# Kernel tuning notes

Measured on AMD Instinct MI355X. Metric: run time of the kernel, lower is better.

The kernel has to match this reference:

```python
import jax, jax.numpy as jnp
import numpy as np
from jax import lax

B, D, N, K, POOL = 256, 512, 50000, 32, 1024
ALPHA, BETA, LAMB = 1.0, 1.0, 1e-4
TAU, EPS, DELTA = 0.1, 0.1, 1e-3
SINKHORN_ITERS = 200


def matrix_sqrt(A):
    # differentiable symmetric PSD matrix sqrt via eigendecomposition
    w, v = jnp.linalg.eigh(A)
    w = jnp.clip(w, 0.0)
    return (v * jnp.sqrt(w)) @ v.T


def ridge_cov(M, delta):
    Dm = M.shape[0]
    S = M + (jnp.trace(M) / Dm * delta) * jnp.eye(Dm, dtype=M.dtype)
    return 0.5 * (S + S.T)


def sinkhorn(p, q, C, eps):
    # entropic OT, fixed-iteration Sinkhorn (ot.sinkhorn equivalent)
    Kmat = jnp.exp(-C / eps)
    def step(uv, _):
        u, v = uv
        u = p / (Kmat @ v + 1e-16)
        v = q / (Kmat.T @ u + 1e-16)
        return (u, v), None
    (u, v), _ = lax.scan(step, (jnp.ones_like(p), jnp.ones_like(q)), None, length=SINKHORN_ITERS)
    return u[:, None] * Kmat * v[None, :]


def setup_inputs():
    key = jax.random.key(0)
    k1, k2, k3, k4, k5, k6 = jax.random.split(key, 6)
    return {
        "q_batch": jax.random.normal(k1, (B, D), jnp.float32),
        "q_indices": jax.random.randint(k2, (B,), 0, POOL),
        "W": jax.random.normal(k3, (D, D), jnp.float32) * 0.05,
        "X": jax.random.normal(k4, (N, D), jnp.float32),
        "pre_indices": jax.random.randint(k5, (POOL, K), 0, N),
        "pre_weights": jax.random.uniform(k6, (POOL, K), jnp.float32, 0.1, 1.0),
    }


def _forward(q_batch, W, X, pre_weights, q_indices, pre_indices):
    T = q_batch @ W  # model := single linear layer, T_q_batch [B, D]
    # ---- distribution alignment (2-Wasserstein between Gaussians) ----
    mu_X = X.mean(0)
    Sigma_X = ridge_cov(jnp.cov(X, rowvar=False).astype(X.dtype), DELTA)
    mu_t = T.mean(0)
    Sigma_t = ridge_cov(jnp.cov(T, rowvar=False).astype(T.dtype), max(DELTA, 1e-4))
    term_mean = jnp.sum((mu_t - mu_X) ** 2)
    s_t = matrix_sqrt(Sigma_t)
    M = s_t @ Sigma_X @ s_t
    s_m = matrix_sqrt(0.5 * (M + M.T))
    term_cov = jnp.trace(Sigma_X + Sigma_t - 2.0 * s_m)
    loss_dist = term_mean + jnp.clip(term_cov, 0.0)
    # ---- kNN consistency with entropic OT ----
    T_sg = lax.stop_gradient(T)  # faiss search is on detached queries
    d2 = (T_sg ** 2).sum(1, keepdims=True) - 2.0 * T_sg @ X.T + (X ** 2).sum(1)[None, :]
    _, post_idx = lax.top_k(-d2, K)  # exact brute-force kNN == faiss IndexFlatL2
    Xn = X[post_idx]  # [B, K, D]
    l2 = ((T[:, None, :] - Xn) ** 2).sum(-1)  # [B, K], grads flow through T
    post_w = jax.nn.softmax(-l2 / TAU, axis=1)
    post_w = jnp.clip(post_w, 1e-8)
    post_w = post_w / post_w.sum(1, keepdims=True)
    pre_idx_b = pre_indices[q_indices]  # [B, K]
    pre_w = jnp.clip(pre_weights[q_indices], 1e-8)
    pre_w = pre_w / pre_w.sum(1, keepdims=True)
    # fixed-size support = concat(pre, post) of size 2K; duplicated points cost 0
    # to move between, so OT value matches the deduped-union formulation
    support = jnp.concatenate([pre_idx_b, post_idx], axis=1)  # [B, 2K]
    S = X[support]  # [B, 2K, D]
    sq = (S ** 2).sum(-1)
    C = jnp.clip(sq[:, :, None] + sq[:, None, :] - 2.0 * jnp.einsum('bid,bjd->bij', S, S), 0.0)
    med = jnp.median(C.reshape(C.shape[0], -1), axis=1)
    C = C / (med[:, None, None] + 1e-8)
    zeros = jnp.zeros_like(pre_w)
    p = jnp.concatenate([pre_w, zeros], axis=1)   # pre mass on first K slots
    q = jnp.concatenate([zeros, post_w], axis=1)  # post mass on last K slots
    plans = jax.vmap(lambda pp, qq, cc: sinkhorn(pp, qq, cc, EPS))(p, q, C)
    loss_knn = (plans * C).sum((1, 2)).mean()
    loss_reg = 0.5 * jnp.sum(W ** 2)
    total = ALPHA * loss_dist + BETA * loss_knn + LAMB * loss_reg
    return total, loss_dist, loss_knn


def reference(q_batch, q_indices, W, X, pre_indices, pre_weights):
    return _forward(q_batch, W, X, pre_weights, q_indices, pre_indices)
```

## Files before the change

### kernel.cpp

```cpp
#include <hip/hip_runtime.h>
#include <float.h>
#include <math.h>

#define BB 256
#define DD 512
#define NN 50000
#define KK 32
#define NS_ITERS 11
#define PARTS 8
#define PCH 6250

#define OFF_G     0
#define OFF_SC    262144
#define OFF_CS    262208
#define OFF_CSS   262720
#define ZERO_F    263232
#define OFF_T     263232
#define OFF_TC    394304
#define OFF_P     525376
#define OFF_H     656448
#define OFF_XSQ   723008
#define OFF_RUNI  781200
#define OFF_PW    789392
#define OFF_PRW   797584
#define OFF_D2    805776

#define OFF_UUT   (OFF_G)
#define OFF_TCTC  (OFF_G + 65536)
#define OFF_W     (OFF_G + 131072)
#define OFF_M     (OFF_G + 131328)
#define OFF_MUT   (OFF_G + 200000)

typedef __attribute__((ext_vector_type(8))) short bf16x8;
typedef __attribute__((ext_vector_type(4))) float f32x4;

__device__ __forceinline__ float waveSum(float v) {
#pragma unroll
  for (int off = 32; off > 0; off >>= 1) v += __shfl_xor(v, off);
  return v;
}

__device__ __forceinline__ void cvt_write(float4 v, unsigned short* hi, unsigned short* lo, int sa) {
  unsigned int b0 = __float_as_uint(v.x), b1 = __float_as_uint(v.y);
  unsigned int b2 = __float_as_uint(v.z), b3 = __float_as_uint(v.w);
  unsigned int h0 = b0 & 0xffff0000u, h1 = b1 & 0xffff0000u;
  unsigned int h2 = b2 & 0xffff0000u, h3 = b3 & 0xffff0000u;
  float l0 = v.x - __uint_as_float(h0), l1 = v.y - __uint_as_float(h1);
  float l2 = v.z - __uint_as_float(h2), l3 = v.w - __uint_as_float(h3);
  *(unsigned int*)&hi[sa]     = (h0 >> 16) | h1;
  *(unsigned int*)&hi[sa + 2] = (h2 >> 16) | h3;
  *(unsigned int*)&lo[sa]     = (__float_as_uint(l0) >> 16) | (__float_as_uint(l1) & 0xffff0000u);
  *(unsigned int*)&lo[sa + 2] = (__float_as_uint(l2) >> 16) | (__float_as_uint(l3) & 0xffff0000u);
}

__device__ __forceinline__ void cvt1(float x, unsigned short* hp, unsigned short* lp) {
// ... 150 lines not shown
      }
#pragma unroll
      for (int nj = 0; nj < 4; ++nj) {
        int ro = (n0 + nj * 16 + lrow) * 72 + kb;
        bh[nj] = *(const bf16x8*)&Bh[ro];
        bl[nj] = *(const bf16x8*)&Bl[ro];
      }
#pragma unroll
      for (int mi = 0; mi < 4; ++mi)
#pragma unroll
        for (int nj = 0; nj < 4; ++nj) {
          acc[mi][nj] = __builtin_amdgcn_mfma_f32_16x16x32_bf16(ah[mi], bh[nj], acc[mi][nj], 0, 0, 0);
          acc[mi][nj] = __builtin_amdgcn_mfma_f32_16x16x32_bf16(ah[mi], bl[nj], acc[mi][nj], 0, 0, 0);
          acc[mi][nj] = __builtin_amdgcn_mfma_f32_16x16x32_bf16(al[mi], bh[nj], acc[mi][nj], 0, 0, 0);
        }
    }
    __syncthreads();
  }
  if (t < 128) colpart[t] = 0.f;
  __syncthreads();
#pragma unroll
  for (int mi = 0; mi < 4; ++mi)
#pragma unroll
    for (int nj = 0; nj < 4; ++nj)
#pragma unroll
      for (int r = 0; r < 4; ++r) {
        int row = bi * 128 + m0 + mi * 16 + lq * 4 + r;
        int col = bj * 128 + n0 + nj * 16 + lrow;
        if (col < NN) V[(size_t)row * NN + col] = acc[mi][nj][r];
      }
#pragma unroll
  for (int nj = 0; nj < 4; ++nj) {
    float s = 0.f;
#pragma unroll
    for (int mi = 0; mi < 4; ++mi)
#pragma unroll
      for (int r = 0; r < 4; ++r) s += acc[mi][nj][r];
    atomicAdd(&colpart[n0 + nj * 16 + lrow], s);
  }
  __syncthreads();
  if (t < 128) {
    int col = bj * 128 + t;
    if (col < NN) atomicAdd(&m[col], colpart[t] * (1.0f / 256.0f));
  }
}

__global__ void __launch_bounds__(256) k_uut(const float* __restrict__ V,
                                             const float* __restrict__ m,
                                             float* __restrict__ UUT) {
  __shared__ unsigned short Ah[128 * 72], Al[128 * 72], Bh[128 * 72], Bl[128 * 72];
  __shared__ __align__(16) float ms[1000];
  const int pi_[3] = {0, 0, 1}, pj_[3] = {0, 1, 1};
  int bi = pi_[blockIdx.x], bj = pj_[blockIdx.x];
  int j0 = blockIdx.y * 1000, jlim = j0 + 1000;
  int t = threadIdx.x;
  int wave = t >> 6, lane = t & 63;
  int m0 = (wave >> 1) * 64, n0 = (wave & 1) * 64;
  int lrow = lane & 15, lq = lane >> 4;
  int r_ = t >> 4, c4_ = (t & 15) * 4;
  f32x4 acc[4][4] = {};
  if (t < 250) ((float4*)ms)[t] = *(const float4*)&m[j0 + t * 4];
  float4 pa[8], pb[8];
#pragma unroll
  for (int f = 0; f < 8; ++f) {
    int r = f * 16 + r_;
    int jb = j0 + c4_;
    float4 va = {0.f, 0.f, 0.f, 0.f}, vb = {0.f, 0.f, 0.f, 0.f};
    if (jb < jlim) {
      va = *(const float4*)&V[(size_t)(bi * 128 + r) * NN + jb];
      vb = *(const float4*)&V[(size_t)(bj * 128 + r) * NN + jb];
    }
    pa[f] = va; pb[f] = vb;
  }
  __syncthreads();
  for (int ch = 0; ch < 16; ++ch) {
    int jc = j0 + ch * 64;
#pragma unroll
    for (int f = 0; f < 8; ++f) {
      int sa = (f * 16 + r_) * 72 + c4_;
      int jb = jc + c4_;
      float4 va = pa[f], vb = pb[f];
      if (jb < jlim) {
        float4 mm = *(const float4*)&ms[jb - j0];
        va.x -= mm.x; va.y -= mm.y; va.z -= mm.z; va.w -= mm.w;
        vb.x -= mm.x; vb.y -= mm.y; vb.z -= mm.z; vb.w -= mm.w;
      }
      cvt_write(va, Ah, Al, sa);
      cvt_write(vb, Bh, Bl, sa);
    }
    __syncthreads();
    if (ch < 15) {
      int jn = j0 + (ch + 1) * 64;
#pragma unroll
      for (int f = 0; f < 8; ++f) {
        int r = f * 16 + r_;
        int jb = jn + c4_;
        float4 va = {0.f, 0.f, 0.f, 0.f}, vb = {0.f, 0.f, 0.f, 0.f};
        if (jb < jlim) {
          va = *(const float4*)&V[(size_t)(bi * 128 + r) * NN + jb];
          vb = *(const float4*)&V[(size_t)(bj * 128 + r) * NN + jb];
        }
        pa[f] = va; pb[f] = vb;
      }
    }
#pragma unroll
    for (int ks = 0; ks < 2; ++ks) {
      int kb = ks * 32 + lq * 8;
      bf16x8 ah[4], al[4], bh[4], bl[4];
#pragma unroll
      for (int mi = 0; mi < 4; ++mi) {
        int ro = (m0 + mi * 16 + lrow) * 72 + kb;
        ah[mi] = *(const bf16x8*)&Ah[ro];
        al[mi] = *(const bf16x8*)&Al[ro];
      }
#pragma unroll
      for (int nj = 0; nj < 4; ++nj) {
        int ro = (n0 + nj * 16 + lrow) * 72 + kb;
        bh[nj] = *(const bf16x8*)&Bh[ro];
        bl[nj] = *(const bf16x8*)&Bl[ro];
      }
#pragma unroll
      for (int mi = 0; mi < 4; ++mi)
#pragma unroll
        for (int nj = 0; nj < 4; ++nj) {
          acc[mi][nj] = __builtin_amdgcn_mfma_f32_16x16x32_bf16(ah[mi], bh[nj], acc[mi][nj], 0, 0, 0);
          acc[mi][nj] = __builtin_amdgcn_mfma_f32_16x16x32_bf16(ah[mi], bl[nj], acc[mi][nj], 0, 0, 0);
          acc[mi][nj] = __builtin_amdgcn_mfma_f32_16x16x32_bf16(al[mi], bh[nj], acc[mi][nj], 0, 0, 0);
        }
    }
    __syncthreads();
  }
#pragma unroll
  for (int mi = 0; mi < 4; ++mi)
#pragma unroll
    for (int nj = 0; nj < 4; ++nj)
#pragma unroll
      for (int r = 0; r < 4; ++r) {
        int row = bi * 128 + m0 + mi * 16 + lq * 4 + r;
        int col = bj * 128 + n0 + nj * 16 + lrow;
        atomicAdd(&UUT[row * 256 + col], acc[mi][nj][r]);
      }
}

__global__ void __launch_bounds__(256) k_colstatX(const float* __restrict__ X, float* __restrict__ colsum,
                                                  float* __restrict__ colss, float* __restrict__ xsq) {
  __shared__ float shs[512], shq[512];
  int b = blockIdx.x, t = threadIdx.x;
  int wave = t >> 6, lane = t & 63;
  shs[t] = 0.f; shq[t] = 0.f; shs[t + 256] = 0.f; shq[t + 256] = 0.f;
  __syncthreads();
  int c0 = lane * 4;
  float s0 = 0, s1 = 0, s2 = 0, s3 = 0, s4 = 0, s5 = 0, s6 = 0, s7 = 0;
  float q0 = 0, q1 = 0, q2 = 0, q3 = 0, q4 = 0, q5 = 0, q6 = 0, q7 = 0;
  int r0 = b * 200 + wave * 50;
  for (int rr = 0; rr < 50; ++rr) {
    const float* Xr = X + (size_t)(r0 + rr) * 512;
    float4 a = *(const float4*)&Xr[c0];
    float4 c = *(const float4*)&Xr[c0 + 256];
    s0 += a.x; s1 += a.y; s2 += a.z; s3 += a.w;
    s4 += c.x; s5 += c.y; s6 += c.z; s7 += c.w;
    float ax = a.x * a.x, ay = a.y * a.y, az = a.z * a.z, aw = a.w * a.w;
    float cx = c.x * c.x, cy = c.y * c.y, cz = c.z * c.z, cw = c.w * c.w;
    q0 += ax; q1 += ay; q2 += az; q3 += aw;
    q4 += cx; q5 += cy; q6 += cz; q7 += cw;
    float rsq = waveSum(((ax + ay) + (az + aw)) + ((cx + cy) + (cz + cw)));
    if (lane == 0) xsq[r0 + rr] = rsq;
  }
  atomicAdd(&shs[c0 + 0], s0); atomicAdd(&shs[c0 + 1], s1);
  atomicAdd(&shs[c0 + 2], s2); atomicAdd(&shs[c0 + 3], s3);
  atomicAdd(&shs[c0 + 256], s4); atomicAdd(&shs[c0 + 257], s5);
  atomicAdd(&shs[c0 + 258], s6); atomicAdd(&shs[c0 + 259], s7);
  atomicAdd(&shq[c0 + 0], q0); atomicAdd(&shq[c0 + 1], q1);
// ... 67 lines not shown
  int l = blockIdx.x * 256 + threadIdx.x;
  int i = l >> 8, j = l & 255;
  float u = (i >= 128 && j < 128) ? UUT[j * 256 + i] : UUT[i * 256 + j];
  float rho = scal[1] * (1e-3f / 512.0f);
  float wm = scal[6] * (1.0f / 256.0f);
  float wi = w[i] - wm, wj = w[j] - wm;
  H[l] = (u - 50000.0f * wi * wj) * (1.0f / (49999.0f * 255.0f))
       + rho * TcTc[i * 256 + j] * (1.0f / 255.0f);
}

__global__ void __launch_bounds__(256) k_power(const float* __restrict__ H,
                                               float* __restrict__ scal) {
  __shared__ float v[256], nv[256], red[4];
  int t = threadIdx.x;
  float rt = scal[0] * (1.0f / 255.0f) * (1e-3f / 512.0f);
  v[t] = 1.0f;
  __syncthreads();
  float n2 = 256.0f, n3 = 256.0f;
  for (int it = 0; it < 3; ++it) {
    float s = rt * v[t];
    for (int j = 0; j < 256; ++j) s += H[j * 256 + t] * v[j];
    nv[t] = s;
    float ss = waveSum(s * s);
    if ((t & 63) == 0) red[t >> 6] = ss;
    __syncthreads();
    float norm2 = red[0] + red[1] + red[2] + red[3];
    if (it == 1) n2 = norm2;
    if (it == 2) n3 = norm2;
    v[t] = nv[t];
    __syncthreads();
  }
  float d = H[t * 256 + t] + rt;
#pragma unroll
  for (int off = 32; off > 0; off >>= 1) d = fmaxf(d, __shfl_xor(d, off));
  if ((t & 63) == 0) red[t >> 6] = d;
  __syncthreads();
  if (t == 0) {
    float lam = sqrtf(n3 / n2);
    float md = fmaxf(fmaxf(red[0], red[1]), fmaxf(red[2], red[3]));
    scal[5] = fmaxf(1.3f * lam, md);
  }
}

__global__ void k_nsinit(const float* __restrict__ H, const float* __restrict__ scal,
                         float* __restrict__ Y, float* __restrict__ Z) {
  int l = blockIdx.x * 256 + threadIdx.x;
  int i = l >> 8, j = l & 255;
  float rt = scal[0] * (1.0f / 255.0f) * (1e-3f / 512.0f);
  float inv = 1.0f / scal[5];
  Y[l] = (H[l] + ((i == j) ? rt : 0.f)) * inv;
  Z[l] = (i == j) ? 1.0f : 0.f;
}

__global__ void __launch_bounds__(256) k_nsp(const float* __restrict__ Z,
                                             const float* __restrict__ Y,
                                             float* __restrict__ P) {
  __shared__ unsigned short Ah[64 * 72], Al[64 * 72], Bh[64 * 72], Bl[64 * 72];
  int n0b = blockIdx.x * 64, m0b = blockIdx.y * 64;
  int t = threadIdx.x, wave = t >> 6, lane = t & 63;
  int m0 = (wave >> 1) * 32, n0 = (wave & 1) * 32;
  int lrow = lane & 15, lq = lane >> 4;
  f32x4 acc[2][2] = {};
  for (int k0 = 0; k0 < 256; k0 += 64) {
#pragma unroll
    for (int f = 0; f < 4; ++f) {
      int lin = f * 256 + t;
      int r = lin >> 4, c4 = (lin & 15) * 4;
      float4 va = *(const float4*)&Z[(m0b + r) * 256 + k0 + c4];
      cvt_write(va, Ah, Al, r * 72 + c4);
      float4 vb = *(const float4*)&Y[(k0 + r) * 256 + n0b + c4];
      cvt1(vb.x, &Bh[(c4 + 0) * 72 + r], &Bl[(c4 + 0) * 72 + r]);
      cvt1(vb.y, &Bh[(c4 + 1) * 72 + r], &Bl[(c4 + 1) * 72 + r]);
      cvt1(vb.z, &Bh[(c4 + 2) * 72 + r], &Bl[(c4 + 2) * 72 + r]);
      cvt1(vb.w, &Bh[(c4 + 3) * 72 + r], &Bl[(c4 + 3) * 72 + r]);
    }
    __syncthreads();
#pragma unroll
    for (int ks = 0; ks < 2; ++ks) {
      int kb = ks * 32 + lq * 8;
      bf16x8 ah[2], al2[2], bh[2], bl2[2];
#pragma unroll
      for (int mi = 0; mi < 2; ++mi) {
        int ro = (m0 + mi * 16 + lrow) * 72 + kb;
        ah[mi] = *(const bf16x8*)&Ah[ro];
        al2[mi] = *(const bf16x8*)&Al[ro];
      }
#pragma unroll
      for (int nj = 0; nj < 2; ++nj) {
        int ro = (n0 + nj * 16 + lrow) * 72 + kb;
        bh[nj] = *(const bf16x8*)&Bh[ro];
        bl2[nj] = *(const bf16x8*)&Bl[ro];
      }
#pragma unroll
      for (int mi = 0; mi < 2; ++mi)
#pragma unroll
        for (int nj = 0; nj < 2; ++nj) {
          acc[mi][nj] = __builtin_amdgcn_mfma_f32_16x16x32_bf16(ah[mi], bh[nj], acc[mi][nj], 0, 0, 0);
          acc[mi][nj] = __builtin_amdgcn_mfma_f32_16x16x32_bf16(ah[mi], bl2[nj], acc[mi][nj], 0, 0, 0);
          acc[mi][nj] = __builtin_amdgcn_mfma_f32_16x16x32_bf16(al2[mi], bh[nj], acc[mi][nj], 0, 0, 0);
        }
    }
    __syncthreads();
  }
#pragma unroll
  for (int mi = 0; mi < 2; ++mi)
#pragma unroll
    for (int nj = 0; nj < 2; ++nj)
#pragma unroll
      for (int r = 0; r < 4; ++r) {
        int row = m0b + m0 + mi * 16 + lq * 4 + r;
        int col = n0b + n0 + nj * 16 + lrow;
        P[row * 256 + col] = acc[mi][nj][r];
      }
}

__global__ void __launch_bounds__(256) k_nsu(const float* __restrict__ Y, const float* __restrict__ Z,
                                             const float* __restrict__ Pm,
                                             float* __restrict__ Yn, float* __restrict__ Zn) {
  __shared__ unsigned short Ah[64 * 72], Al[64 * 72], Bh[64 * 72], Bl[64 * 72];
  int zz = blockIdx.z;
  const float* A = zz ? Pm : Y;
  const float* B = zz ? Z : Pm;
  const float* D = zz ? Z : Y;
  float* O = zz ? Zn : Yn;
  int n0b = blockIdx.x * 64, m0b = blockIdx.y * 64;
  int t = threadIdx.x, wave = t >> 6, lane = t & 63;
  int m0 = (wave >> 1) * 32, n0 = (wave & 1) * 32;
  int lrow = lane & 15, lq = lane >> 4;
  f32x4 acc[2][2] = {};
  for (int k0 = 0; k0 < 256; k0 += 64) {
#pragma unroll
    for (int f = 0; f < 4; ++f) {
      int lin = f * 256 + t;
      int r = lin >> 4, c4 = (lin & 15) * 4;
      float4 va = *(const float4*)&A[(m0b + r) * 256 + k0 + c4];
      cvt_write(va, Ah, Al, r * 72 + c4);
      float4 vb = *(const float4*)&B[(k0 + r) * 256 + n0b + c4];
      cvt1(vb.x, &Bh[(c4 + 0) * 72 + r], &Bl[(c4 + 0) * 72 + r]);
      cvt1(vb.y, &Bh[(c4 + 1) * 72 + r], &Bl[(c4 + 1) * 72 + r]);
      cvt1(vb.z, &Bh[(c4 + 2) * 72 + r], &Bl[(c4 + 2) * 72 + r]);
      cvt1(vb.w, &Bh[(c4 + 3) * 72 + r], &Bl[(c4 + 3) * 72 + r]);
    }
    __syncthreads();
#pragma unroll
    for (int ks = 0; ks < 2; ++ks) {
      int kb = ks * 32 + lq * 8;
      bf16x8 ah[2], al2[2], bh[2], bl2[2];
#pragma unroll
      for (int mi = 0; mi < 2; ++mi) {
        int ro = (m0 + mi * 16 + lrow) * 72 + kb;
        ah[mi] = *(const bf16x8*)&Ah[ro];
        al2[mi] = *(const bf16x8*)&Al[ro];
      }
#pragma unroll
      for (int nj = 0; nj < 2; ++nj) {
        int ro = (n0 + nj * 16 + lrow) * 72 + kb;
        bh[nj] = *(const bf16x8*)&Bh[ro];
        bl2[nj] = *(const bf16x8*)&Bl[ro];
      }
#pragma unroll
      for (int mi = 0; mi < 2; ++mi)
#pragma unroll
        for (int nj = 0; nj < 2; ++nj) {
          acc[mi][nj] = __builtin_amdgcn_mfma_f32_16x16x32_bf16(ah[mi], bh[nj], acc[mi][nj], 0, 0, 0);
          acc[mi][nj] = __builtin_amdgcn_mfma_f32_16x16x32_bf16(ah[mi], bl2[nj], acc[mi][nj], 0, 0, 0);
          acc[mi][nj] = __builtin_amdgcn_mfma_f32_16x16x32_bf16(al2[mi], bh[nj], acc[mi][nj], 0, 0, 0);
        }
    }
    __syncthreads();
  }
#pragma unroll
  for (int mi = 0; mi < 2; ++mi)
#pragma unroll
    for (int nj = 0; nj < 2; ++nj)
#pragma unroll
      for (int r = 0; r < 4; ++r) {
        int row = m0b + m0 + mi * 16 + lq * 4 + r;
        int col = n0b + n0 + nj * 16 + lrow;
        int idx = row * 256 + col;
        O[idx] = 1.5f * D[idx] - 0.5f * acc[mi][nj][r];
      }
}

__global__ void k_ns_trace(const float* __restrict__ Y, float* __restrict__ scal) {
  __shared__ float red[4];
  int t = threadIdx.x;
  float v = Y[t * 256 + t];
  v = waveSum(v);
  if ((t & 63) == 0) red[t >> 6] = v;
  __syncthreads();
  if (t == 0) {
    float tr = red[0] + red[1] + red[2] + red[3];
    float rt = scal[0] * (1.0f / 255.0f) * (1e-3f / 512.0f);
    scal[2] = sqrtf(scal[5]) * tr + 256.0f * sqrtf(rt);
  }
}

__global__ void __launch_bounds__(256) k_topk_part(const float* __restrict__ V,
                                                   const float* __restrict__ xsq,
                                                   float* __restrict__ candv,
                                                   int* __restrict__ candi) {
  __shared__ float bufv[512];
  __shared__ int bufi[512];
  __shared__ int lcount;
  __shared__ float tvs;
  __shared__ int tis;
  int part = blockIdx.x, q = blockIdx.y, t = threadIdx.x;
  int base = part * PCH;
  int lane = t & 63;
  if (t == 0) { lcount = 0; tvs = FLT_MAX; tis = 0x7fffffff; }
  __syncthreads();
  const float* rowV = V + (size_t)q * NN + base;
  const float* xs = xsq + base;

  auto flush = [&]() {
    __syncthreads();
    int c = lcount;
    for (int s = c + t; s < 512; s += 256) { bufv[s] = FLT_MAX; bufi[s] = 0x7fffffff; }
    __syncthreads();
    for (int ssz = 2; ssz <= 512; ssz <<= 1) {
      for (int st = ssz >> 1; st > 0; st >>= 1) {
        int i = 2 * t - (t & (st - 1));
        int j = i + st;
        bool up = ((i & ssz) == 0);
        float a = bufv[i], b = bufv[j];
        int ai = bufi[i], bi2 = bufi[j];
        bool agtb = (a > b) || (a == b && ai > bi2);
        if (agtb == up) { bufv[i] = b; bufv[j] = a; bufi[i] = bi2; bufi[j] = ai; }
        __syncthreads();
      }
    }
    if (t == 0) { lcount = 32; tvs = bufv[31]; tis = bufi[31]; }
    __syncthreads();
  };

  int ntile = (PCH + 255) >> 8;
  for (int tile = 0; tile < ntile; ++tile) {
    int j = tile * 256 + t;
    float val = 0.f; int idx = 0;
    bool pred = false;
    if (j < PCH) {
      val = xs[j] - 2.0f * rowV[j];
      idx = base + j;
      float tv = tvs; int ti = tis;
      pred = (val < tv) || (val == tv && idx < ti);
    }
    unsigned long long mask = __ballot(pred);
// ... 50 lines not shown
                                                const float* __restrict__ prew, float* __restrict__ postw,
                                                float* __restrict__ prewn) {
  __shared__ float l2s[32];
  int b = blockIdx.x, t = threadIdx.x;
  int wave = t >> 6, lane = t & 63;
  int qi = qidx[b];
  if (wave == 0) {
    float pwv = (lane < 32) ? fmaxf(prew[qi * 32 + lane], 1e-8f) : 0.f;
    float psum = waveSum(pwv);
    if (lane < 32) prewn[b * 32 + lane] = pwv / psum;
  }
  const float* Tb = T + b * 512;
#pragma unroll
  for (int n8 = 0; n8 < 8; ++n8) {
    int n = wave * 8 + n8;
    int nb = runi[b * 32 + n];
    const float* Xr = X + (size_t)nb * 512;
    float acc = 0.f;
#pragma unroll
    for (int d = 0; d < 8; ++d) {
      float df = Tb[lane + 64 * d] - Xr[lane + 64 * d];
      acc += df * df;
    }
    acc = waveSum(acc);
    if (lane == 0) l2s[n] = acc;
  }
  __syncthreads();
  if (wave == 0) {
    float lg = (lane < 32) ? (-l2s[lane] * 10.0f) : -FLT_MAX;
    float mx = lg;
#pragma unroll
    for (int off = 32; off > 0; off >>= 1) mx = fmaxf(mx, __shfl_xor(mx, off));
    float e = (lane < 32) ? expf(lg - mx) : 0.f;
    float es = waveSum(e);
    float wv = e / es;
    wv = fmaxf(wv, 1e-8f);
    float ws2 = (lane < 32) ? wv : 0.f;
    ws2 = waveSum(ws2);
    if (lane < 32) postw[b * 32 + lane] = wv / ws2;
  }
}

__global__ void __launch_bounds__(256) k_batch(const float* __restrict__ X, const int* __restrict__ qidx,
                                               const int* __restrict__ pre_idx, const int* __restrict__ runi,
                                               const float* __restrict__ prewn, const float* __restrict__ postw,
                                               float* __restrict__ scal) {
  __shared__ float G[64][65];
  __shared__ float Cm[64][65];
  __shared__ unsigned short Ah[64 * 72], Al[64 * 72];
  __shared__ int supp[64];
  __shared__ float uuS[32], vvS[32];
  __shared__ float red[4];
  __shared__ float medsh;
  __shared__ unsigned int cw[4], mw[4];
  int b = blockIdx.x, t = threadIdx.x;
  int wave = t >> 6, lane = t & 63;
  if (t < 32) supp[t] = pre_idx[qidx[b] * 32 + t];
  else if (t < 64) supp[t] = runi[b * 32 + t - 32];
  __syncthreads();
  {
    int m0 = (wave >> 1) * 32, n0 = (wave & 1) * 32;
    int lrow = lane & 15, lq = lane >> 4;
    int r_ = t >> 4, c4_ = (t & 15) * 4;
    f32x4 acc[2][2] = {};
    float4 pf[4];
#pragma unroll
    for (int f = 0; f < 4; ++f) {
      int r = f * 16 + r_;
      pf[f] = *(const float4*)&X[(size_t)supp[r] * 512 + c4_];
    }
    for (int kc = 0; kc < 512; kc += 64) {
#pragma unroll
      for (int f = 0; f < 4; ++f)
        cvt_write(pf[f], Ah, Al, (f * 16 + r_) * 72 + c4_);
      __syncthreads();
      if (kc < 448) {
        int kn = kc + 64;
#pragma unroll
        for (int f = 0; f < 4; ++f) {
          int r = f * 16 + r_;
          pf[f] = *(const float4*)&X[(size_t)supp[r] * 512 + kn + c4_];
        }
      }
#pragma unroll
      for (int ks = 0; ks < 2; ++ks) {
        int kb = ks * 32 + lq * 8;
        bf16x8 ah[2], al[2], bh[2], bl[2];
#pragma unroll
        for (int mi = 0; mi < 2; ++mi) {
          int ro = (m0 + mi * 16 + lrow) * 72 + kb;
          ah[mi] = *(const bf16x8*)&Ah[ro];
          al[mi] = *(const bf16x8*)&Al[ro];
        }
#pragma unroll
        for (int nj = 0; nj < 2; ++nj) {
          int ro = (n0 + nj * 16 + lrow) * 72 + kb;
          bh[nj] = *(const bf16x8*)&Ah[ro];
          bl[nj] = *(const bf16x8*)&Al[ro];
        }
#pragma unroll
        for (int mi = 0; mi < 2; ++mi)
#pragma unroll
          for (int nj = 0; nj < 2; ++nj) {
            acc[mi][nj] = __builtin_amdgcn_mfma_f32_16x16x32_bf16(ah[mi], bh[nj], acc[mi][nj], 0, 0, 0);
            acc[mi][nj] = __builtin_amdgcn_mfma_f32_16x16x32_bf16(ah[mi], bl[nj], acc[mi][nj], 0, 0, 0);
            acc[mi][nj] = __builtin_amdgcn_mfma_f32_16x16x32_bf16(al[mi], bh[nj], acc[mi][nj], 0, 0, 0);
          }
      }
      __syncthreads();
    }
#pragma unroll
    for (int mi = 0; mi < 2; ++mi)
#pragma unroll
      for (int nj = 0; nj < 2; ++nj)
#pragma unroll
        for (int r = 0; r < 4; ++r)
          G[m0 + mi * 16 + lq * 4 + r][n0 + nj * 16 + lrow] = acc[mi][nj][r];
  }
  __syncthreads();
  unsigned int uval[16];
#pragma unroll
  for (int s = 0; s < 16; ++s) {
    int l = s * 256 + t;
    int i = l >> 6, j = l & 63;
    float cc = fmaxf(G[i][i] + G[j][j] - 2.0f * G[i][j], 0.f);
    Cm[i][j] = cc;
    uval[s] = (i < j) ? (__float_as_uint(cc) & 0x7fffffffu) : 0xffffffffu;
  }
  unsigned int ans = 0;
  for (int bb = 30; bb >= 0; --bb) {
    unsigned int test = ans | (1u << bb);
    int cw_ = 0;
#pragma unroll
    for (int s = 0; s < 16; ++s)
      cw_ += __popcll(__ballot(uval[s] < test));
    __syncthreads();
    if (lane == 0) red[wave] = (float)cw_;
    __syncthreads();
    int cnt = (int)(red[0] + red[1] + red[2] + red[3]);
    if (cnt < 992) ans = test;
  }
  {
    unsigned int target = ans;
    unsigned int cnt = 0, mn = 0xffffffffu;
#pragma unroll
    for (int s = 0; s < 16; ++s) {
      unsigned int u = uval[s];
      if (u <= target) cnt++;
      else mn = (u < mn) ? u : mn;
    }
#pragma unroll
    for (int off = 32; off > 0; off >>= 1) {
      cnt += __shfl_xor(cnt, off);
      unsigned int m2 = __shfl_xor(mn, off);
      mn = (m2 < mn) ? m2 : mn;
    }
    __syncthreads();
    if (lane == 0) { cw[wave] = cnt; mw[wave] = mn; }
    __syncthreads();
    if (t == 0) {
      unsigned int ct = cw[0] + cw[1] + cw[2] + cw[3];
      unsigned int mt = mw[0];
      mt = (mw[1] < mt) ? mw[1] : mt;
      mt = (mw[2] < mt) ? mw[2] : mt;
      mt = (mw[3] < mt) ? mw[3] : mt;
      float v992 = __uint_as_float(target);
      float v993 = (ct >= 993u) ? v992 : __uint_as_float(mt);
      medsh = 0.5f * (v992 + v993) + 1e-8f;
    }
    __syncthreads();
  }
  float inv = 1.0f / medsh;
  for (int l = t; l < 4096; l += 256) {
    int i = l >> 6, j = l & 63;
    float cn = Cm[i][j] * inv;
    Cm[i][j] = cn;
    G[i][j] = expf(-cn * 10.0f);
  }
  __syncthreads();
  if (wave == 0) {
    int half = lane >> 5;
    int l = lane & 31;
    int cb = half * 16;
    float p_l = prewn[b * 32 + l];
    float q_l = postw[b * 32 + l];
    float Kr16[16], Kt16[16];
#pragma unroll
    for (int c2 = 0; c2 < 16; ++c2) Kr16[c2] = G[l][32 + cb + c2];
#pragma unroll
    for (int r2 = 0; r2 < 16; ++r2) Kt16[r2] = G[cb + r2][32 + l];
    float r0 = 0.f;
#pragma unroll
    for (int c2 = 0; c2 < 32; ++c2) r0 += G[l][half * 32 + c2];
    r0 += __shfl_xor(r0, 32);
    float u = p_l / (r0 + 1e-16f);
    float s0 = 0.f, s1 = 0.f, s2 = 0.f, s3 = 0.f;
#pragma unroll
    for (int r2 = 0; r2 < 16; r2 += 4) {
      s0 += Kt16[r2]     * __shfl(u, cb + r2);
      s1 += Kt16[r2 + 1] * __shfl(u, cb + r2 + 1);
      s2 += Kt16[r2 + 2] * __shfl(u, cb + r2 + 2);
      s3 += Kt16[r2 + 3] * __shfl(u, cb + r2 + 3);
    }
    float sv = (s0 + s1) + (s2 + s3);
    sv += __shfl_xor(sv, 32);
    float v = q_l / (sv + 1e-16f);
    float pu = u, pv = v;
    float ppu = 0.f, ppv = 0.f;
    for (int it = 1; it < 200; ++it) {
      float a0 = 0.f, a1 = 0.f, a2 = 0.f, a3 = 0.f;
#pragma unroll
      for (int c2 = 0; c2 < 16; c2 += 4) {
        a0 += Kr16[c2]     * __shfl(v, cb + c2);
        a1 += Kr16[c2 + 1] * __shfl(v, cb + c2 + 1);
        a2 += Kr16[c2 + 2] * __shfl(v, cb + c2 + 2);
        a3 += Kr16[c2 + 3] * __shfl(v, cb + c2 + 3);
      }
      float au = (a0 + a1) + (a2 + a3);
      au += __shfl_xor(au, 32);
      u = p_l / (au + 1e-16f);
      a0 = 0.f; a1 = 0.f; a2 = 0.f; a3 = 0.f;
#pragma unroll
      for (int r2 = 0; r2 < 16; r2 += 4) {
        a0 += Kt16[r2]     * __shfl(u, cb + r2);
        a1 += Kt16[r2 + 1] * __shfl(u, cb + r2 + 1);
        a2 += Kt16[r2 + 2] * __shfl(u, cb + r2 + 2);
        a3 += Kt16[r2 + 3] * __shfl(u, cb + r2 + 3);
      }
      float bv = (a0 + a1) + (a2 + a3);
      bv += __shfl_xor(bv, 32);
      v = q_l / (bv + 1e-16f);
      if (__all(u == pu && v == pv)) break;
      if (it >= 2 && __all(u == ppu && v == ppv)) {
        if ((199 - it) & 1) { u = pu; v = pv; }
        break;
      }
      ppu = pu; ppv = pv; pu = u; pv = v;
    }
    if (t < 32) { uuS[t] = u; vvS[t] = v; }
  }
  __syncthreads();
  float lacc = 0.f;
#pragma unroll
  for (int q8 = 0; q8 < 4; ++q8) {
    int l = q8 * 256 + t;
    int i = l >> 5, j = l & 31;
    lacc += uuS[i] * G[i][32 + j] * vvS[j] * Cm[i][32 + j];
  }
  lacc = waveSum(lacc);
  if ((t & 63) == 0) red[t >> 6] = lacc;
  __syncthreads();
  if (t == 0)
    atomicAdd(&scal[3], (red[0] + red[1] + red[2] + red[3]) * (1.0f / 256.0f));
}

__global__ void k_wreg(const float* __restrict__ W, float* __restrict__ scal) {
  __shared__ float red[4];
  int t = threadIdx.x;
  int base = blockIdx.x * 2048;
  float ss = 0.f;
#pragma unroll
  for (int p = 0; p < 8; ++p) {
    float v = W[base + p * 256 + t];
    ss += v * v;
  }
  ss = waveSum(ss);
  if ((t & 63) == 0) red[t >> 6] = ss;
  __syncthreads();
  if (t == 0) atomicAdd(&scal[4], red[0] + red[1] + red[2] + red[3]);
}

__global__ void k_combine(const float* __restrict__ mu_t, const float* __restrict__ colsum,
                          const float* __restrict__ scal, float* __restrict__ out) {
  __shared__ float red[8];
  int t = threadIdx.x;
  float dm = mu_t[t] * (1.0f / 256.0f) - colsum[t] * (1.0f / 50000.0f);
  float v = dm * dm;
  v = waveSum(v);
  if ((t & 63) == 0) red[t >> 6] = v;
  __syncthreads();
  if (t == 0) {
    float term_mean = 0.f;
    for (int i = 0; i < 8; ++i) term_mean += red[i];
    float trCT = scal[0] * (1.0f / 255.0f);
    float trCX = scal[1];
    float S = scal[2];
    float term_cov = trCX * 1.001f + trCT * 1.001f - 2.0f * S;
    term_cov = fmaxf(term_cov, 0.f);
    float loss_dist = term_mean + term_cov;
    float loss_knn = scal[3];
    float loss_reg = 0.5f * scal[4];
    out[0] = loss_dist + loss_knn + 1e-4f * loss_reg;
    out[1] = loss_dist;
    out[2] = loss_knn;
  }
}

extern "C" void kernel_launch(void* const* d_in, const int* in_sizes, int n_in,
                              void* d_out, int out_size, void* d_ws, size_t ws_size,
                              hipStream_t stream) {
  const float* q = (const float*)d_in[0];
  const int* qidx = (const int*)d_in[1];
  const float* W = (const float*)d_in[2];
  const float* X = (const float*)d_in[3];
  const int* pre_idx = (const int*)d_in[4];
  const float* prew = (const float*)d_in[5];
  float* out = (float*)d_out;
  float* ws = (float*)d_ws;

  float* scal = ws + OFF_SC;
  float* colsum = ws + OFF_CS;
  float* colss = ws + OFF_CSS;
  float* T = ws + OFF_T;
  float* Tc = ws + OFF_TC;
  float* H = ws + OFF_H;
  float* mu_t = ws + OFF_MUT;
  float* xsq = ws + OFF_XSQ;
  int* runi = (int*)(ws + OFF_RUNI);
  float* postw = ws + OFF_PW;
  float* prewn = ws + OFF_PRW;
  float* V = ws + OFF_D2;
  float* UUT = ws + OFF_UUT;
  float* TcTc = ws + OFF_TCTC;
  float* wv = ws + OFF_W;
  float* m = ws + OFF_M;
  float* candv = ws + OFF_P;
  int* candi = (int*)(ws + OFF_P + 65536);

  hipMemsetAsync(d_ws, 0, (size_t)ZERO_F * 4, stream);

  k_g64_nn<<<dim3(8, 4), 256, 0, stream>>>(q, W, T, 512, 512, 512, 512, 1.0f, mu_t);
  k_colstatX<<<250, 256, 0, stream>>>(X, colsum, colss, xsq);
  k_centerT<<<128, 256, 0, stream>>>(T, mu_t, Tc, scal);
  k_trCX<<<1, 512, 0, stream>>>(colsum, colss, scal);
  k_vgemm<<<dim3(391, 2), 256, 0, stream>>>(T, X, V, m);
  k_topk_part<<<dim3(PARTS, 256), 256, 0, stream>>>(V, xsq, candv, candi);
  k_topk_final<<<256, 128, 0, stream>>>(candv, candi, runi);
  k_g64_nt<<<dim3(4, 4), 256, 0, stream>>>(Tc, Tc, TcTc, 512, 512, 512, 256, 1.0f);
  k_wvec<<<8, 256, 0, stream>>>(T, colsum, wv, scal);
  k_uut<<<dim3(3, 50), 256, 0, stream>>>(V, m, UUT);
  k_hfix<<<256, 256, 0, stream>>>(UUT, TcTc, wv, scal, H);
  {
    float* Y = ws + OFF_TC;
    float* Z = ws + OFF_TC + 65536;
    float* Y2 = ws + OFF_P;
    float* Z2 = ws + OFF_P + 65536;
    float* Pm = ws + OFF_G;
    k_power<<<1, 256, 0, stream>>>(H, scal);
    k_nsinit<<<256, 256, 0, stream>>>(H, scal, Y, Z);
    for (int it = 0; it < NS_ITERS; ++it) {
      k_nsp<<<dim3(4, 4), 256, 0, stream>>>(Z, Y, Pm);
      k_nsu<<<dim3(4, 4, 2), 256, 0, stream>>>(Y, Z, Pm, Y2, Z2);
      float* tmp = Y; Y = Y2; Y2 = tmp;
      tmp = Z; Z = Z2; Z2 = tmp;
    }
    k_ns_trace<<<1, 256, 0, stream>>>(Y, scal);
  }
  k_l2soft<<<256, 256, 0, stream>>>(T, X, runi, qidx, prew, postw, prewn);
  k_batch<<<256, 256, 0, stream>>>(X, qidx, pre_idx, runi, prewn, postw, scal);
  k_wreg<<<128, 256, 0, stream>>>(W, scal);
  k_combine<<<1, 512, 0, stream>>>(mu_t, colsum, scal, out);
}
```

Baseline: 905.3 us.

## Fuse Newton-Schulz chain into cooperative kernel, dedupe diagonal UUT tiles, simplify median

The H construction, power iteration, Newton-Schulz init, all iterations and the trace are merged into one cooperative kernel of 32 blocks that uses grid.sync instead of roughly 25 separate launches. The last iteration updates only the diagonal Y tiles, since only the trace is needed. Separately, diagonal tiles of the UUT Gram kernel reuse the A operand instead of loading and converting V twice. The per-batch median search is moved onto a single wave, which removes block barriers but leaves the other waves idle. Grid syncs carry their own cost, and the cooperative path relies on device support, with the old launch sequence kept as a fallback.

```diff
diff --git a/kernel.cpp b/kernel.cpp
--- a/kernel.cpp
+++ b/kernel.cpp
@@ -1,6 +1,9 @@
 #include <hip/hip_runtime.h>
+#include <hip/hip_cooperative_groups.h>
 #include <float.h>
 #include <math.h>
+
+namespace cg = cooperative_groups;
 
 #define BB 256
 #define DD 512
@@ -257,6 +260,7 @@
   __shared__ __align__(16) float ms[1000];
   const int pi_[3] = {0, 0, 1}, pj_[3] = {0, 1, 1};
   int bi = pi_[blockIdx.x], bj = pj_[blockIdx.x];
+  bool diag = (bi == bj);
   int j0 = blockIdx.y * 1000, jlim = j0 + 1000;
   int t = threadIdx.x;
   int wave = t >> 6, lane = t & 63;
@@ -273,11 +277,13 @@
     float4 va = {0.f, 0.f, 0.f, 0.f}, vb = {0.f, 0.f, 0.f, 0.f};
     if (jb < jlim) {
       va = *(const float4*)&V[(size_t)(bi * 128 + r) * NN + jb];
-      vb = *(const float4*)&V[(size_t)(bj * 128 + r) * NN + jb];
+      if (!diag) vb = *(const float4*)&V[(size_t)(bj * 128 + r) * NN + jb];
     }
     pa[f] = va; pb[f] = vb;
   }
   __syncthreads();
+  const unsigned short* BhP = diag ? (const unsigned short*)Ah : (const unsigned short*)Bh;
+  const unsigned short* BlP = diag ? (const unsigned short*)Al : (const unsigned short*)Bl;
   for (int ch = 0; ch < 16; ++ch) {
     int jc = j0 + ch * 64;
 #pragma unroll
@@ -288,10 +294,10 @@
       if (jb < jlim) {
         float4 mm = *(const float4*)&ms[jb - j0];
         va.x -= mm.x; va.y -= mm.y; va.z -= mm.z; va.w -= mm.w;
-        vb.x -= mm.x; vb.y -= mm.y; vb.z -= mm.z; vb.w -= mm.w;
+        if (!diag) { vb.x -= mm.x; vb.y -= mm.y; vb.z -= mm.z; vb.w -= mm.w; }
       }
       cvt_write(va, Ah, Al, sa);
-      cvt_write(vb, Bh, Bl, sa);
+      if (!diag) cvt_write(vb, Bh, Bl, sa);
     }
     __syncthreads();
     if (ch < 15) {
@@ -303,7 +309,7 @@
         float4 va = {0.f, 0.f, 0.f, 0.f}, vb = {0.f, 0.f, 0.f, 0.f};
         if (jb < jlim) {
           va = *(const float4*)&V[(size_t)(bi * 128 + r) * NN + jb];
-          vb = *(const float4*)&V[(size_t)(bj * 128 + r) * NN + jb];
+          if (!diag) vb = *(const float4*)&V[(size_t)(bj * 128 + r) * NN + jb];
         }
         pa[f] = va; pb[f] = vb;
       }
@@ -321,8 +327,8 @@
 #pragma unroll
       for (int nj = 0; nj < 4; ++nj) {
         int ro = (n0 + nj * 16 + lrow) * 72 + kb;
-        bh[nj] = *(const bf16x8*)&Bh[ro];
-        bl[nj] = *(const bf16x8*)&Bl[ro];
+        bh[nj] = *(const bf16x8*)&BhP[ro];
+        bl[nj] = *(const bf16x8*)&BlP[ro];
       }
 #pragma unroll
       for (int mi = 0; mi < 4; ++mi)
@@ -496,78 +502,11 @@
   Z[l] = (i == j) ? 1.0f : 0.f;
 }
 
-__global__ void __launch_bounds__(256) k_nsp(const float* __restrict__ Z,
-                                             const float* __restrict__ Y,
-                                             float* __restrict__ P) {
-  __shared__ unsigned short Ah[64 * 72], Al[64 * 72], Bh[64 * 72], Bl[64 * 72];
-  int n0b = blockIdx.x * 64, m0b = blockIdx.y * 64;
-  int t = threadIdx.x, wave = t >> 6, lane = t & 63;
-  int m0 = (wave >> 1) * 32, n0 = (wave & 1) * 32;
-  int lrow = lane & 15, lq = lane >> 4;
-  f32x4 acc[2][2] = {};
-  for (int k0 = 0; k0 < 256; k0 += 64) {
-#pragma unroll
-    for (int f = 0; f < 4; ++f) {
-      int lin = f * 256 + t;
-      int r = lin >> 4, c4 = (lin & 15) * 4;
-      float4 va = *(const float4*)&Z[(m0b + r) * 256 + k0 + c4];
-      cvt_write(va, Ah, Al, r * 72 + c4);
-      float4 vb = *(const float4*)&Y[(k0 + r) * 256 + n0b + c4];
-      cvt1(vb.x, &Bh[(c4 + 0) * 72 + r], &Bl[(c4 + 0) * 72 + r]);
-      cvt1(vb.y, &Bh[(c4 + 1) * 72 + r], &Bl[(c4 + 1) * 72 + r]);
-      cvt1(vb.z, &Bh[(c4 + 2) * 72 + r], &Bl[(c4 + 2) * 72 + r]);
-      cvt1(vb.w, &Bh[(c4 + 3) * 72 + r], &Bl[(c4 + 3) * 72 + r]);
-    }
-    __syncthreads();
-#pragma unroll
-    for (int ks = 0; ks < 2; ++ks) {
-      int kb = ks * 32 + lq * 8;
-      bf16x8 ah[2], al2[2], bh[2], bl2[2];
-#pragma unroll
-      for (int mi = 0; mi < 2; ++mi) {
-        int ro = (m0 + mi * 16 + lrow) * 72 + kb;
-        ah[mi] = *(const bf16x8*)&Ah[ro];
-        al2[mi] = *(const bf16x8*)&Al[ro];
-      }
-#pragma unroll
-      for (int nj = 0; nj < 2; ++nj) {
-        int ro = (n0 + nj * 16 + lrow) * 72 + kb;
-        bh[nj] = *(const bf16x8*)&Bh[ro];
-        bl2[nj] = *(const bf16x8*)&Bl[ro];
-      }
-#pragma unroll
-      for (int mi = 0; mi < 2; ++mi)
-#pragma unroll
-        for (int nj = 0; nj < 2; ++nj) {
-          acc[mi][nj] = __builtin_amdgcn_mfma_f32_16x16x32_bf16(ah[mi], bh[nj], acc[mi][nj], 0, 0, 0);
-          acc[mi][nj] = __builtin_amdgcn_mfma_f32_16x16x32_bf16(ah[mi], bl2[nj], acc[mi][nj], 0, 0, 0);
-          acc[mi][nj] = __builtin_amdgcn_mfma_f32_16x16x32_bf16(al2[mi], bh[nj], acc[mi][nj], 0, 0, 0);
-        }
-    }
-    __syncthreads();
-  }
-#pragma unroll
-  for (int mi = 0; mi < 2; ++mi)
-#pragma unroll
-    for (int nj = 0; nj < 2; ++nj)
-#pragma unroll
-      for (int r = 0; r < 4; ++r) {
-        int row = m0b + m0 + mi * 16 + lq * 4 + r;
-        int col = n0b + n0 + nj * 16 + lrow;
-        P[row * 256 + col] = acc[mi][nj][r];
-      }
-}
-
-__global__ void __launch_bounds__(256) k_nsu(const float* __restrict__ Y, const float* __restrict__ Z,
-                                             const float* __restrict__ Pm,
-                                             float* __restrict__ Yn, float* __restrict__ Zn) {
-  __shared__ unsigned short Ah[64 * 72], Al[64 * 72], Bh[64 * 72], Bl[64 * 72];
-  int zz = blockIdx.z;
-  const float* A = zz ? Pm : Y;
-  const float* B = zz ? Z : Pm;
-  const float* D = zz ? Z : Y;
-  float* O = zz ? Zn : Yn;
-  int n0b = blockIdx.x * 64, m0b = blockIdx.y * 64;
+__device__ __forceinline__ void ns_mfma_tile(const float* __restrict__ A, const float* __restrict__ B,
+                                             const float* __restrict__ D, float* __restrict__ O,
+                                             int m0b, int n0b, float dscale, float ascale,
+                                             unsigned short* Ah, unsigned short* Al,
+                                             unsigned short* Bh, unsigned short* Bl) {
   int t = threadIdx.x, wave = t >> 6, lane = t & 63;
   int m0 = (wave >> 1) * 32, n0 = (wave & 1) * 32;
   int lrow = lane & 15, lq = lane >> 4;
@@ -622,8 +561,27 @@
         int row = m0b + m0 + mi * 16 + lq * 4 + r;
         int col = n0b + n0 + nj * 16 + lrow;
         int idx = row * 256 + col;
-        O[idx] = 1.5f * D[idx] - 0.5f * acc[mi][nj][r];
-      }
+        float base = (dscale != 0.f) ? dscale * D[idx] : 0.f;
+        O[idx] = base + ascale * acc[mi][nj][r];
+      }
+}
+
+__global__ void __launch_bounds__(256) k_nsp(const float* __restrict__ Z,
+                                             const float* __restrict__ Y,
+                                             float* __restrict__ P) {
+  __shared__ unsigned short Ah[64 * 72], Al[64 * 72], Bh[64 * 72], Bl[64 * 72];
+  ns_mfma_tile(Z, Y, Z, P, blockIdx.y * 64, blockIdx.x * 64, 0.f, 1.0f, Ah, Al, Bh, Bl);
+}
+
+__global__ void __launch_bounds__(256) k_nsu(const float* __restrict__ Y, const float* __restrict__ Z,
+                                             const float* __restrict__ Pm,
+                                             float* __restrict__ Yn, float* __restrict__ Zn) {
+  __shared__ unsigned short Ah[64 * 72], Al[64 * 72], Bh[64 * 72], Bl[64 * 72];
+  int zz = blockIdx.z;
+  if (zz == 0)
+    ns_mfma_tile(Y, Pm, Y, Yn, blockIdx.y * 64, blockIdx.x * 64, 1.5f, -0.5f, Ah, Al, Bh, Bl);
+  else
+    ns_mfma_tile(Pm, Z, Z, Zn, blockIdx.y * 64, blockIdx.x * 64, 1.5f, -0.5f, Ah, Al, Bh, Bl);
 }
 
 __global__ void k_ns_trace(const float* __restrict__ Y, float* __restrict__ scal) {
@@ -637,6 +595,115 @@
     float tr = red[0] + red[1] + red[2] + red[3];
     float rt = scal[0] * (1.0f / 255.0f) * (1e-3f / 512.0f);
     scal[2] = sqrtf(scal[5]) * tr + 256.0f * sqrtf(rt);
+  }
+}
+
+__global__ void __launch_bounds__(256) k_nsall(const float* __restrict__ UUT,
+                                               const float* __restrict__ TcTc,
+                                               const float* __restrict__ w,
+                                               float* __restrict__ scal,
+                                               float* __restrict__ H,
+                                               float* __restrict__ Y, float* __restrict__ Z,
+                                               float* __restrict__ Y2, float* __restrict__ Z2,
+                                               float* __restrict__ Pm) {
+  cg::grid_group grid = cg::this_grid();
+  __shared__ unsigned short Ah[64 * 72], Al[64 * 72], Bh[64 * 72], Bl[64 * 72];
+  __shared__ float pv[256], pnv[256], red2[4];
+  int t = threadIdx.x, blk = blockIdx.x;
+  {
+    float rho = scal[1] * (1e-3f / 512.0f);
+    float wm = scal[6] * (1.0f / 256.0f);
+#pragma unroll
+    for (int e = 0; e < 8; ++e) {
+      int l = blk * 2048 + e * 256 + t;
+      int i = l >> 8, j = l & 255;
+      float u = (i >= 128 && j < 128) ? UUT[j * 256 + i] : UUT[i * 256 + j];
+      float wi = w[i] - wm, wj = w[j] - wm;
+      H[l] = (u - 50000.0f * wi * wj) * (1.0f / (49999.0f * 255.0f))
+           + rho * TcTc[i * 256 + j] * (1.0f / 255.0f);
+    }
+  }
+  grid.sync();
+  if (blk == 0) {
+    float rt = scal[0] * (1.0f / 255.0f) * (1e-3f / 512.0f);
+    pv[t] = 1.0f;
+    __syncthreads();
+    float n2 = 256.0f, n3 = 256.0f;
+    for (int it2 = 0; it2 < 3; ++it2) {
+      float s = rt * pv[t];
+      for (int j = 0; j < 256; ++j) s += H[j * 256 + t] * pv[j];
+      pnv[t] = s;
+      float ss = waveSum(s * s);
+      if ((t & 63) == 0) red2[t >> 6] = ss;
+      __syncthreads();
+      float norm2 = red2[0] + red2[1] + red2[2] + red2[3];
+      if (it2 == 1) n2 = norm2;
+      if (it2 == 2) n3 = norm2;
+      pv[t] = pnv[t];
+      __syncthreads();
+    }
+    float d = H[t * 256 + t] + rt;
+#pragma unroll
+    for (int off = 32; off > 0; off >>= 1) d = fmaxf(d, __shfl_xor(d, off));
+    if ((t & 63) == 0) red2[t >> 6] = d;
+    __syncthreads();
+    if (t == 0) {
+      float lam = sqrtf(n3 / n2);
+      float md = fmaxf(fmaxf(red2[0], red2[1]), fmaxf(red2[2], red2[3]));
+      scal[5] = fmaxf(1.3f * lam, md);
+    }
+  }
+  grid.sync();
+  {
+    float rt = scal[0] * (1.0f / 255.0f) * (1e-3f / 512.0f);
+    float inv = 1.0f / scal[5];
+#pragma unroll
+    for (int e = 0; e < 8; ++e) {
+      int l = blk * 2048 + e * 256 + t;
+      int i = l >> 8, j = l & 255;
+      Y[l] = (H[l] + ((i == j) ? rt : 0.f)) * inv;
+      Z[l] = (i == j) ? 1.0f : 0.f;
+    }
+  }
+  grid.sync();
+  for (int it = 0; it < NS_ITERS; ++it) {
+    const float* Yc = (it & 1) ? Y2 : Y;
+    const float* Zc = (it & 1) ? Z2 : Z;
+    float* Yn = (it & 1) ? Y : Y2;
+    float* Zn = (it & 1) ? Z : Z2;
+    if (blk < 16) {
+      int bi = blk >> 2, bj = blk & 3;
+      ns_mfma_tile(Zc, Yc, Zc, Pm, bi * 64, bj * 64, 0.f, 1.0f, Ah, Al, Bh, Bl);
+    }
+    grid.sync();
+    if (it < NS_ITERS - 1) {
+      if (blk < 16) {
+        int bi = blk >> 2, bj = blk & 3;
+        ns_mfma_tile(Yc, Pm, Yc, Yn, bi * 64, bj * 64, 1.5f, -0.5f, Ah, Al, Bh, Bl);
+      } else {
+        int j = blk - 16;
+        int bi = j >> 2, bj = j & 3;
+        ns_mfma_tile(Pm, Zc, Zc, Zn, bi * 64, bj * 64, 1.5f, -0.5f, Ah, Al, Bh, Bl);
+      }
+    } else {
+      if (blk < 16) {
+        int bi = blk >> 2, bj = blk & 3;
+        if (bi == bj)
+          ns_mfma_tile(Yc, Pm, Yc, Yn, bi * 64, bj * 64, 1.5f, -0.5f, Ah, Al, Bh, Bl);
+      }
+    }
+    grid.sync();
+  }
+  if (blk == 0) {
+    float v = Y2[t * 256 + t];
+    v = waveSum(v);
+    if ((t & 63) == 0) red2[t >> 6] = v;
+    __syncthreads();
+    if (t == 0) {
+      float tr = red2[0] + red2[1] + red2[2] + red2[3];
+      float rt = scal[0] * (1.0f / 255.0f) * (1e-3f / 512.0f);
+      scal[2] = sqrtf(scal[5]) * tr + 256.0f * sqrtf(rt);
+    }
   }
 }
 
@@ -793,7 +860,6 @@
   __shared__ float uuS[32], vvS[32];
   __shared__ float red[4];
   __shared__ float medsh;
-  __shared__ unsigned int cw[4], mw[4];
   int b = blockIdx.x, t = threadIdx.x;
   int wave = t >> 6, lane = t & 63;
   if (t < 32) supp[t] = pre_idx[qidx[b] * 32 + t];
@@ -859,58 +925,45 @@
           G[m0 + mi * 16 + lq * 4 + r][n0 + nj * 16 + lrow] = acc[mi][nj][r];
   }
   __syncthreads();
-  unsigned int uval[16];
-#pragma unroll
-  for (int s = 0; s < 16; ++s) {
-    int l = s * 256 + t;
+  for (int l = t; l < 4096; l += 256) {
     int i = l >> 6, j = l & 63;
-    float cc = fmaxf(G[i][i] + G[j][j] - 2.0f * G[i][j], 0.f);
-    Cm[i][j] = cc;
-    uval[s] = (i < j) ? (__float_as_uint(cc) & 0x7fffffffu) : 0xffffffffu;
-  }
-  unsigned int ans = 0;
-  for (int bb = 30; bb >= 0; --bb) {
-    unsigned int test = ans | (1u << bb);
-    int cw_ = 0;
-#pragma unroll
-    for (int s = 0; s < 16; ++s)
-      cw_ += __popcll(__ballot(uval[s] < test));
-    __syncthreads();
-    if (lane == 0) red[wave] = (float)cw_;
-    __syncthreads();
-    int cnt = (int)(red[0] + red[1] + red[2] + red[3]);
-    if (cnt < 992) ans = test;
-  }
-  {
-    unsigned int target = ans;
-    unsigned int cnt = 0, mn = 0xffffffffu;
-#pragma unroll
-    for (int s = 0; s < 16; ++s) {
-      unsigned int u = uval[s];
-      if (u <= target) cnt++;
-      else mn = (u < mn) ? u : mn;
+    Cm[i][j] = fmaxf(G[i][i] + G[j][j] - 2.0f * G[i][j], 0.f);
+  }
+  __syncthreads();
+  if (wave == 0) {
+    unsigned int uv2[64];
+#pragma unroll
+    for (int s = 0; s < 64; ++s)
+      uv2[s] = (s < lane) ? (__float_as_uint(Cm[s][lane]) & 0x7fffffffu) : 0xffffffffu;
+    unsigned int ans = 0;
+    for (int bb2 = 30; bb2 >= 0; --bb2) {
+      unsigned int test = ans | (1u << bb2);
+      int cnt = 0;
+#pragma unroll
+      for (int s = 0; s < 64; ++s)
+        cnt += __popcll(__ballot(uv2[s] < test));
+      if (cnt < 992) ans = test;
+    }
+    unsigned int cnt2 = 0, mn = 0xffffffffu;
+#pragma unroll
+    for (int s = 0; s < 64; ++s) {
+      unsigned int u2 = uv2[s];
+      if (u2 <= ans) cnt2++;
+      else mn = (u2 < mn) ? u2 : mn;
     }
 #pragma unroll
     for (int off = 32; off > 0; off >>= 1) {
-      cnt += __shfl_xor(cnt, off);
+      cnt2 += __shfl_xor(cnt2, off);
       unsigned int m2 = __shfl_xor(mn, off);
       mn = (m2 < mn) ? m2 : mn;
     }
-    __syncthreads();
-    if (lane == 0) { cw[wave] = cnt; mw[wave] = mn; }
-    __syncthreads();
-    if (t == 0) {
-      unsigned int ct = cw[0] + cw[1] + cw[2] + cw[3];
-      unsigned int mt = mw[0];
-      mt = (mw[1] < mt) ? mw[1] : mt;
-      mt = (mw[2] < mt) ? mw[2] : mt;
-      mt = (mw[3] < mt) ? mw[3] : mt;
-      float v992 = __uint_as_float(target);
-      float v993 = (ct >= 993u) ? v992 : __uint_as_float(mt);
+    if (lane == 0) {
+      float v992 = __uint_as_float(ans);
+      float v993 = (cnt2 >= 993u) ? v992 : __uint_as_float(mn);
       medsh = 0.5f * (v992 + v993) + 1e-8f;
     }
-    __syncthreads();
-  }
+  }
+  __syncthreads();
   float inv = 1.0f / medsh;
   for (int l = t; l < 4096; l += 256) {
     int i = l >> 6, j = l & 63;
@@ -946,7 +999,7 @@
     float sv = (s0 + s1) + (s2 + s3);
     sv += __shfl_xor(sv, 32);
     float v = q_l / (sv + 1e-16f);
-    float pu = u, pv = v;
+    float pu = u, pv2 = v;
     float ppu = 0.f, ppv = 0.f;
     for (int it = 1; it < 200; ++it) {
       float a0 = 0.f, a1 = 0.f, a2 = 0.f, a3 = 0.f;
@@ -971,12 +1024,12 @@
       float bv = (a0 + a1) + (a2 + a3);
       bv += __shfl_xor(bv, 32);
       v = q_l / (bv + 1e-16f);
-      if (__all(u == pu && v == pv)) break;
+      if (__all(u == pu && v == pv2)) break;
       if (it >= 2 && __all(u == ppu && v == ppv)) {
-        if ((199 - it) & 1) { u = pu; v = pv; }
+        if ((199 - it) & 1) { u = pu; v = pv2; }
         break;
       }
-      ppu = pu; ppv = pv; pu = u; pv = v;
+      ppu = pu; ppv = pv2; pu = u; pv2 = v;
     }
     if (t < 32) { uuS[t] = u; vvS[t] = v; }
   }
@@ -1080,22 +1133,36 @@
   k_g64_nt<<<dim3(4, 4), 256, 0, stream>>>(Tc, Tc, TcTc, 512, 512, 512, 256, 1.0f);
   k_wvec<<<8, 256, 0, stream>>>(T, colsum, wv, scal);
   k_uut<<<dim3(3, 50), 256, 0, stream>>>(V, m, UUT);
-  k_hfix<<<256, 256, 0, stream>>>(UUT, TcTc, wv, scal, H);
   {
     float* Y = ws + OFF_TC;
     float* Z = ws + OFF_TC + 65536;
     float* Y2 = ws + OFF_P;
     float* Z2 = ws + OFF_P + 65536;
     float* Pm = ws + OFF_G;
-    k_power<<<1, 256, 0, stream>>>(H, scal);
-    k_nsinit<<<256, 256, 0, stream>>>(H, scal, Y, Z);
-    for (int it = 0; it < NS_ITERS; ++it) {
-      k_nsp<<<dim3(4, 4), 256, 0, stream>>>(Z, Y, Pm);
-      k_nsu<<<dim3(4, 4, 2), 256, 0, stream>>>(Y, Z, Pm, Y2, Z2);
-      float* tmp = Y; Y = Y2; Y2 = tmp;
-      tmp = Z; Z = Z2; Z2 = tmp;
-    }
-    k_ns_trace<<<1, 256, 0, stream>>>(Y, scal);
+    static int coopOK = -1;
+    if (coopOK < 0) {
+      int v = 0;
+      if (hipDeviceGetAttribute(&v, hipDeviceAttributeCooperativeLaunch, 0) != hipSuccess) v = 0;
+      coopOK = v;
+    }
+    if (coopOK) {
+      const float* a_uut = UUT; const float* a_tctc = TcTc; const float* a_w = wv;
+      float* a_scal = scal; float* a_H = H;
+      float* aY = Y; float* aZ = Z; float* aY2 = Y2; float* aZ2 = Z2; float* aPm = Pm;
+      void* kargs[] = {&a_uut, &a_tctc, &a_w, &a_scal, &a_H, &aY, &aZ, &aY2, &aZ2, &aPm};
+      hipLaunchCooperativeKernel((const void*)k_nsall, dim3(32), dim3(256), kargs, 0, stream);
+    } else {
+      k_hfix<<<256, 256, 0, stream>>>(UUT, TcTc, wv, scal, H);
+      k_power<<<1, 256, 0, stream>>>(H, scal);
+      k_nsinit<<<256, 256, 0, stream>>>(H, scal, Y, Z);
+      for (int it = 0; it < NS_ITERS; ++it) {
+        k_nsp<<<dim3(4, 4), 256, 0, stream>>>(Z, Y, Pm);
+        k_nsu<<<dim3(4, 4, 2), 256, 0, stream>>>(Y, Z, Pm, Y2, Z2);
+        float* tmp = Y; Y = Y2; Y2 = tmp;
+        tmp = Z; Z = Z2; Z2 = tmp;
+      }
+      k_ns_trace<<<1, 256, 0, stream>>>(Y, scal);
+    }
   }
   k_l2soft<<<256, 256, 0, stream>>>(T, X, runi, qidx, prew, postw, prewn);
   k_batch<<<256, 256, 0, stream>>>(X, qidx, pre_idx, runi, prewn, postw, scal);
```

After: 971.4 us. 1.07x slower.
